# Kernel optimization log

Hardware: AMD Instinct MI355X
Metric: run time of the kernel (lower is better)

## Reference

```python
import jax, jax.numpy as jnp
import numpy as np

N_NODES = 100000
N_EDGES = 1600000
IN_DIM = 128
HID = 128
OUT = 64


def gcn_conv(x, src, dst, W, b, n_nodes):
    # x: [N, Din] -> [N, Dout]; symmetric-normalized GCN with self-loops (PyG GCNConv defaults)
    h = x @ W  # transform first (as PyG does)
    loop = jnp.arange(n_nodes, dtype=src.dtype)
    s = jnp.concatenate([src, loop])
    d = jnp.concatenate([dst, loop])
    deg = jax.ops.segment_sum(jnp.ones_like(d, dtype=h.dtype), d, num_segments=n_nodes)
    dis = jnp.where(deg > 0, jax.lax.rsqrt(deg), 0.0)
    norm = dis[s] * dis[d]  # [E+N]
    msgs = h[s] * norm[:, None]  # gather-transform
    out = jax.ops.segment_sum(msgs, d, num_segments=n_nodes)  # scatter-add
    return out + b


def setup_inputs() -> dict:
    key = jax.random.key(0)
    ks = jax.random.split(key, 12)
    x = jax.random.normal(ks[0], (N_NODES, IN_DIM), dtype=jnp.float32)
    edge_index = jax.random.randint(ks[1], (2, N_EDGES), 0, N_NODES, dtype=jnp.int32)
    def lin(k, fan_in, fan_out):
        bound = 1.0 / np.sqrt(fan_in)
        kw, kb = jax.random.split(k)
        W = jax.random.uniform(kw, (fan_in, fan_out), minval=-bound, maxval=bound, dtype=jnp.float32)
        b = jax.random.uniform(kb, (fan_out,), minval=-bound, maxval=bound, dtype=jnp.float32)
        return W, b
    W1, b1 = lin(ks[2], IN_DIM, HID)
    W2, b2 = lin(ks[3], HID, HID)
    Wp1, bp1 = lin(ks[4], HID, HID)
    Wp2, bp2 = lin(ks[5], HID, OUT)
    return {"x": x, "edge_index": edge_index,
            "W1": W1, "b1": b1, "W2": W2, "b2": b2,
            "Wp1": Wp1, "bp1": bp1, "Wp2": Wp2, "bp2": bp2}


def reference(x, edge_index, W1, b1, W2, b2, Wp1, bp1, Wp2, bp2):
    n = x.shape[0]
    src, dst = edge_index[0], edge_index[1]
    # layer 1: GCNConv + relu (dropout inactive at eval)
    h = jax.nn.relu(gcn_conv(x, src, dst, W1, b1, n))
    # layer 2
    h = jax.nn.relu(gcn_conv(h, src, dst, W2, b2, n))
    # post MLP head
    h = h @ Wp1 + bp1
    h = h @ Wp2 + bp2
    return jax.nn.log_softmax(h, axis=1)
```

## Files before the change

### kernel.cpp

```cpp
#include <hip/hip_runtime.h>
#include <hip/hip_bf16.h>
#include <cstdint>

typedef __attribute__((ext_vector_type(8))) short short8;
typedef __attribute__((ext_vector_type(16))) float f32x16;
typedef unsigned short us;

#define BIN_SHIFT 9
#define BIN_NODES 512
#define CAPB 12288
#define EPB 4096

__device__ __forceinline__ float bflo(uint32_t u) { return __builtin_bit_cast(float, u << 16); }
__device__ __forceinline__ float bfhi(uint32_t u) { return __builtin_bit_cast(float, u & 0xffff0000u); }

__device__ __forceinline__ us f32_to_bf16_rne(float f) {
  uint32_t u = __builtin_bit_cast(uint32_t, f);
  u += 0x7fffu + ((u >> 16) & 1u);
  return (us)(u >> 16);
}

__device__ __forceinline__ void split2(float f, us& h, us& l) {
  uint32_t u = __builtin_bit_cast(uint32_t, f);
  h = (us)(u >> 16);
  float fh = __builtin_bit_cast(float, u & 0xffff0000u);
  float r = f - fh;
  l = (us)(__builtin_bit_cast(uint32_t, r) >> 16);
}

__global__ __launch_bounds__(256) void k_binA(
    const int* __restrict__ src, const int* __restrict__ dst,
    uint2* __restrict__ binbuf, int* __restrict__ gcur, int E, int nbins) {
  __shared__ uint2 stage[EPB];
  __shared__ int cnt[256], base[256], cur[256], gbase[256];
  int tid = threadIdx.x;
  int e0 = blockIdx.x * EPB;
  int ne = min(EPB, E - e0);
  if (ne <= 0) return;
  cnt[tid] = 0;
  __syncthreads();
  for (int i = tid; i < ne; i += 256) atomicAdd(&cnt[dst[e0 + i] >> BIN_SHIFT], 1);
  __syncthreads();
  if (tid < 64) {
    int carry = 0;
#pragma unroll
    for (int c = 0; c < 4; ++c) {
      int v = cnt[c * 64 + tid];
      int incl = v;
#pragma unroll
      for (int off = 1; off < 64; off <<= 1) {
        int t = __shfl_up(incl, off, 64);
        if (tid >= off) incl += t;
      }
      base[c * 64 + tid] = carry + incl - v;
      carry += __shfl(incl, 63, 64);
    }
  }
  __syncthreads();
  if (tid < nbins && cnt[tid] > 0) gbase[tid] = atomicAdd(&gcur[tid], cnt[tid]);
  cur[tid] = base[tid];
  __syncthreads();
  for (int i = tid; i < ne; i += 256) {
    int d = dst[e0 + i], s = src[e0 + i];
    int p = atomicAdd(&cur[d >> BIN_SHIFT], 1);
    stage[p] = make_uint2((unsigned)d, (unsigned)s);
  }
  __syncthreads();
  for (int i = tid; i < ne; i += 256) {
    uint2 en = stage[i];
    int b = en.x >> BIN_SHIFT;
    int gi = gbase[b] + (i - base[b]);
    if (gi < CAPB) binbuf[(size_t)b * CAPB + gi] = en;
  }
}

__global__ __launch_bounds__(256) void k_passB(
    const uint2* __restrict__ binbuf, const int* __restrict__ gcur,
    int* __restrict__ deg, float* __restrict__ dis, int* __restrict__ start,
    int* __restrict__ col, int N, int nbins) {
  __shared__ int hist[512], lstart[512], cur[512];
  __shared__ int colstage[CAPB];
  __shared__ int binbase_s;
  int b = blockIdx.x, tid = threadIdx.x;
  int node0 = b << BIN_SHIFT;
  int cnt = min(gcur[b], CAPB);
  hist[tid] = 0; hist[tid + 256] = 0;
  __syncthreads();
  const uint2* bp = binbuf + (size_t)b * CAPB;
  for (int i = tid; i < cnt; i += 256) atomicAdd(&hist[bp[i].x & (BIN_NODES - 1)], 1);
  __syncthreads();
  if (tid < 64) {
    int s = 0;
    for (int i = tid; i < b; i += 64) s += min(gcur[i], CAPB);
#pragma unroll
    for (int off = 32; off; off >>= 1) s += __shfl_xor(s, off, 64);
    if (tid == 0) binbase_s = s;
    int carry = 0;
#pragma unroll
    for (int c = 0; c < 8; ++c) {
      int v = hist[c * 64 + tid];
      int incl = v;
#pragma unroll
      for (int off = 1; off < 64; off <<= 1) {
        int t = __shfl_up(incl, off, 64);
        if (tid >= off) incl += t;
      }
      lstart[c * 64 + tid] = carry + incl - v;
      carry += __shfl(incl, 63, 64);
    }
  }
  __syncthreads();
  int binbase = binbase_s;
  for (int i = tid; i < 512; i += 256) {
    int node = node0 + i;
    if (node < N) {
      int dg = hist[i];
      deg[node] = dg;
      dis[node] = rsqrtf((float)(dg + 1));
      start[node] = binbase + lstart[i];
    }
  }
  cur[tid] = lstart[tid]; cur[tid + 256] = lstart[tid + 256];
  __syncthreads();
  for (int i = tid; i < cnt; i += 256) {
    uint2 en = bp[i];
    int p = atomicAdd(&cur[en.x & (BIN_NODES - 1)], 1);
    colstage[p] = (int)en.y;
  }
  __syncthreads();
  for (int i = tid; i < cnt; i += 256) col[binbase + i] = colstage[i];
}

__global__ void k_prep(const float* __restrict__ W1, const float* __restrict__ W2,
                       const float* __restrict__ Wp1, const float* __restrict__ Wp2,
                       const float* __restrict__ bp1, const float* __restrict__ bp2,
                       us* __restrict__ Wt1h, us* __restrict__ Wt1l,
                       us* __restrict__ Wt2h, us* __restrict__ Wt2l,
                       us* __restrict__ Wch, us* __restrict__ Wcl, float* __restrict__ bc) {
  int blk = blockIdx.x, tid = threadIdx.x;
  if (blk < 128) {
    const float* W = (blk < 64) ? W1 : W2;
    us* Wh = (blk < 64) ? Wt1h : Wt2h;
    us* Wl = (blk < 64) ? Wt1l : Wt2l;
    int idx = (blk & 63) * 256 + tid;
    int k = idx >> 7, n = idx & 127;
    us h, l;
    split2(W[idx], h, l);
    Wh[n * 128 + k] = h;
    Wl[n * 128 + k] = l;
  } else if (blk < 160) {
    int idx = (blk - 128) * 256 + tid;
    int k = idx >> 6, j = idx & 63;
    float acc = 0.f;
    for (int t = 0; t < 128; ++t) acc += Wp1[k * 128 + t] * Wp2[t * 64 + j];
    us h, l;
    split2(acc, h, l);
    Wch[j * 128 + k] = h;
    Wcl[j * 128 + k] = l;
  } else {
    int j = tid;
    if (j < 64) {
      float acc = bp2[j];
      for (int t = 0; t < 128; ++t) acc += bp1[t] * Wp2[t * 64 + j];
      bc[j] = acc;
    }
  }
}

template <bool AF32>
__global__ __launch_bounds__(256) void k_gemm_mfma(
    const void* __restrict__ Av, const us* __restrict__ Wh,
    const us* __restrict__ Wl, const float* __restrict__ dis,
    us* __restrict__ out_bf16, int N, int ntiles) {
  __shared__ us As_hi[32 * 136];
  __shared__ us As_lo[32 * 136];
  int tid = threadIdx.x;
  int wave = tid >> 6, lane = tid & 63;
  int n0 = wave * 32;
  int nn = n0 + (lane & 31);
  int khalf = (lane >> 5) * 8;
  int m = lane & 31;

  short8 bh[8], bl[8];
#pragma unroll
  for (int c = 0; c < 8; ++c) {
    bh[c] = *(const short8*)&Wh[nn * 128 + c * 16 + khalf];
    bl[c] = *(const short8*)&Wl[nn * 128 + c * 16 + khalf];
  }

  for (int t = blockIdx.x; t < ntiles; t += gridDim.x) {
    int row0 = t * 32;
    __syncthreads();
    if (AF32) {
      const float* A = (const float*)Av;
      for (int j = tid; j < 1024; j += 256) {
        int r = j >> 5, c = j & 31;
        int row = row0 + r;
        float4 v = make_float4(0.f, 0.f, 0.f, 0.f);
        if (row < N) v = *(const float4*)&A[(size_t)row * 128 + c * 4];
        us h0, h1, h2, h3, l0, l1, l2, l3;
        split2(v.x, h0, l0); split2(v.y, h1, l1);
        split2(v.z, h2, l2); split2(v.w, h3, l3);
        *(ushort4*)&As_hi[r * 136 + c * 4] = make_ushort4(h0, h1, h2, h3);
        *(ushort4*)&As_lo[r * 136 + c * 4] = make_ushort4(l0, l1, l2, l3);
      }
    } else {
      const us* A = (const us*)Av;
      for (int j = tid; j < 512; j += 256) {
        int r = j >> 4, c = j & 15;
        int row = row0 + r;
        uint4 v = make_uint4(0u, 0u, 0u, 0u);
        if (row < N) v = *(const uint4*)&A[(size_t)row * 128 + c * 8];
        *(uint4*)&As_hi[r * 136 + c * 8] = v;
      }
    }
    __syncthreads();

    f32x16 acc = {};
#pragma unroll
    for (int c = 0; c < 8; ++c) {
      short8 ah = *(const short8*)&As_hi[m * 136 + c * 16 + khalf];
      acc = __builtin_amdgcn_mfma_f32_32x32x16_bf16(ah, bh[c], acc, 0, 0, 0);
      acc = __builtin_amdgcn_mfma_f32_32x32x16_bf16(ah, bl[c], acc, 0, 0, 0);
      if (AF32) {
        short8 al = *(const short8*)&As_lo[m * 136 + c * 16 + khalf];
        acc = __builtin_amdgcn_mfma_f32_32x32x16_bf16(al, bh[c], acc, 0, 0, 0);
      }
    }

    int col = n0 + (lane & 31);
    int rbase = row0 + 4 * (lane >> 5);
#pragma unroll
    for (int reg = 0; reg < 16; ++reg) {
      int row = rbase + (reg & 3) + 8 * (reg >> 2);
      if (row < N) {
        float v = acc[reg] * dis[row];
        out_bf16[(size_t)row * 128 + col] = f32_to_bf16_rne(v);
      }
    }
  }
}

__global__ __launch_bounds__(256) void k_gather(
    const us* __restrict__ h, us* __restrict__ o,
    const int* __restrict__ start, const int* __restrict__ deg,
    const int* __restrict__ col, const float* __restrict__ dis,
    const float* __restrict__ bias, int N) {
  int tid = threadIdx.x;
  int node = blockIdx.x * 8 + (tid >> 5);
  int lane = tid & 31;
  if (node >= N) return;
  const uint2* h2 = (const uint2*)h;
  uint2 u = h2[(size_t)node * 32 + lane];
  float ax = bflo(u.x), ay = bfhi(u.x), az = bflo(u.y), aw = bfhi(u.y);
  int e = start[node];
  int e_end = e + deg[node];
  for (; e + 1 < e_end; e += 2) {
    uint2 u1 = h2[(size_t)col[e] * 32 + lane];
    uint2 u2 = h2[(size_t)col[e + 1] * 32 + lane];
    ax += bflo(u1.x) + bflo(u2.x); ay += bfhi(u1.x) + bfhi(u2.x);
    az += bflo(u1.y) + bflo(u2.y); aw += bfhi(u1.y) + bfhi(u2.y);
  }
  if (e < e_end) {
    uint2 u1 = h2[(size_t)col[e] * 32 + lane];
    ax += bflo(u1.x); ay += bfhi(u1.x); az += bflo(u1.y); aw += bfhi(u1.y);
  }
  float sc = dis[node];
  float4 b = ((const float4*)bias)[lane];
  float rx = fmaxf(ax * sc + b.x, 0.f);
  float ry = fmaxf(ay * sc + b.y, 0.f);
  float rz = fmaxf(az * sc + b.z, 0.f);
  float rw = fmaxf(aw * sc + b.w, 0.f);
  uint2 po;
  po.x = ((uint32_t)f32_to_bf16_rne(ry) << 16) | f32_to_bf16_rne(rx);
  po.y = ((uint32_t)f32_to_bf16_rne(rw) << 16) | f32_to_bf16_rne(rz);
  ((uint2*)o)[(size_t)node * 32 + lane] = po;
}

__global__ __launch_bounds__(256) void k_head_mfma(
    const us* __restrict__ act, const us* __restrict__ Wch,
    const us* __restrict__ Wcl, const float* __restrict__ bc,
    float* __restrict__ out, int N) {
  __shared__ us As[64 * 136];
  __shared__ float red[2][2][64];
  int tid = threadIdx.x;
  int wave = tid >> 6, lane = tid & 63;
  int rt = wave >> 1, ct = wave & 1;
  int colj = ct * 32 + (lane & 31);
  int khalf = (lane >> 5) * 8;
  int m = lane & 31;

  short8 bh[8], bl[8];
#pragma unroll
  for (int c = 0; c < 8; ++c) {
    bh[c] = *(const short8*)&Wch[colj * 128 + c * 16 + khalf];
    bl[c] = *(const short8*)&Wcl[colj * 128 + c * 16 + khalf];
  }

  int row0 = blockIdx.x * 64;
  for (int j = tid; j < 1024; j += 256) {
    int r = j >> 4, c = j & 15;
    int row = row0 + r;
    uint4 v = make_uint4(0u, 0u, 0u, 0u);
    if (row < N) v = *(const uint4*)&act[(size_t)row * 128 + c * 8];
    *(uint4*)&As[r * 136 + c * 8] = v;
  }
  __syncthreads();

  f32x16 acc = {};
  int mrow = rt * 32 + m;
#pragma unroll
  for (int c = 0; c < 8; ++c) {
    short8 ah = *(const short8*)&As[mrow * 136 + c * 16 + khalf];
    acc = __builtin_amdgcn_mfma_f32_32x32x16_bf16(ah, bh[c], acc, 0, 0, 0);
    acc = __builtin_amdgcn_mfma_f32_32x32x16_bf16(ah, bl[c], acc, 0, 0, 0);
  }

  float bcv = bc[colj];
  float lg[16], mx[16];
#pragma unroll
  for (int reg = 0; reg < 16; ++reg) {
    lg[reg] = acc[reg] + bcv;
    float v = lg[reg];
#pragma unroll
    for (int off = 16; off > 0; off >>= 1) v = fmaxf(v, __shfl_xor(v, off, 32));
    mx[reg] = v;
  }
  if ((lane & 31) == 0) {
#pragma unroll
    for (int reg = 0; reg < 16; ++reg) {
      int rl = rt * 32 + (reg & 3) + 8 * (reg >> 2) + 4 * (lane >> 5);
      red[0][ct][rl] = mx[reg];
    }
  }
  __syncthreads();

  float ex[16], sm[16];
#pragma unroll
  for (int reg = 0; reg < 16; ++reg) {
    int rl = rt * 32 + (reg & 3) + 8 * (reg >> 2) + 4 * (lane >> 5);
    float rmax = fmaxf(red[0][0][rl], red[0][1][rl]);
    ex[reg] = lg[reg] - rmax;
    float v = expf(ex[reg]);
#pragma unroll
    for (int off = 16; off > 0; off >>= 1) v += __shfl_xor(v, off, 32);
    sm[reg] = v;
  }
  if ((lane & 31) == 0) {
#pragma unroll
    for (int reg = 0; reg < 16; ++reg) {
      int rl = rt * 32 + (reg & 3) + 8 * (reg >> 2) + 4 * (lane >> 5);
      red[1][ct][rl] = sm[reg];
    }
  }
  __syncthreads();

#pragma unroll
  for (int reg = 0; reg < 16; ++reg) {
    int rl = rt * 32 + (reg & 3) + 8 * (reg >> 2) + 4 * (lane >> 5);
    int row = row0 + rl;
    if (row < N) {
      float total = red[1][0][rl] + red[1][1][rl];
      out[(size_t)row * 64 + colj] = ex[reg] - logf(total);
    }
  }
}

extern "C" void kernel_launch(void* const* d_in, const int* in_sizes, int n_in,
                              void* d_out, int out_size, void* d_ws, size_t ws_size,
                              hipStream_t stream) {
  const float* x   = (const float*)d_in[0];
  const int*   ei  = (const int*)d_in[1];
  const float* W1  = (const float*)d_in[2];
  const float* b1  = (const float*)d_in[3];
  const float* W2  = (const float*)d_in[4];
  const float* b2  = (const float*)d_in[5];
  const float* Wp1 = (const float*)d_in[6];
  const float* bp1 = (const float*)d_in[7];
  const float* Wp2 = (const float*)d_in[8];
  const float* bp2 = (const float*)d_in[9];
  float* out = (float*)d_out;

  int N = in_sizes[0] / 128;
  int E = in_sizes[1] / 2;
  const int* src = ei;
  const int* dst = ei + E;
  int nbins = (N + BIN_NODES - 1) >> BIN_SHIFT;

  float* dis   = (float*)d_ws;
  int*   deg   = (int*)(dis + N);
  int*   start = deg + N;
  int*   col   = start + N;
  int*   gcur  = col + ((E + 3) & ~3);
  us* Wt1h = (us*)(gcur + 256);
  us* Wt1l = Wt1h + 16384;
  us* Wt2h = Wt1l + 16384;
  us* Wt2l = Wt2h + 16384;
  us* Wch  = Wt2l + 16384;
  us* Wcl  = Wch + 8192;
  float* bc = (float*)(Wcl + 8192);
  uint2* binbuf = (uint2*)(bc + 80);
  us* hbuf = (us*)(binbuf + (size_t)nbins * CAPB);
  us* act  = hbuf + (size_t)N * 128;

  hipMemsetAsync(gcur, 0, 256 * sizeof(int), stream);

  int ablocks = (E + EPB - 1) / EPB;
  k_binA<<<ablocks, 256, 0, stream>>>(src, dst, binbuf, gcur, E, nbins);
  k_passB<<<nbins, 256, 0, stream>>>(binbuf, gcur, deg, dis, start, col, N, nbins);
  k_prep<<<161, 256, 0, stream>>>(W1, W2, Wp1, Wp2, bp1, bp2,
                                  Wt1h, Wt1l, Wt2h, Wt2l, Wch, Wcl, bc);

  int ntiles = (N + 31) / 32;
  int gemm_grid = ntiles < 1024 ? ntiles : 1024;
  int agblocks = (N + 7) / 8;
  int hblocks = (N + 63) / 64;

  k_gemm_mfma<true><<<gemm_grid, 256, 0, stream>>>(x, Wt1h, Wt1l, dis, hbuf, N, ntiles);
  k_gather<<<agblocks, 256, 0, stream>>>(hbuf, act, start, deg, col, dis, b1, N);
  k_gemm_mfma<false><<<gemm_grid, 256, 0, stream>>>(act, Wt2h, Wt2l, dis, hbuf, N, ntiles);
  k_gather<<<agblocks, 256, 0, stream>>>(hbuf, act, start, deg, col, dis, b2, N);
  k_head_mfma<<<hblocks, 256, 0, stream>>>(act, Wch, Wcl, bc, out, N);
}
```

Baseline: 409.3 us.

## Fuse neighbor aggregation into following GEMM/head kernels and pack bin entries

Fuses the layer-1 gather into the layer-2 MFMA GEMM and the layer-2 gather into the output head kernel, so the aggregated activations go straight into shared memory instead of through a global buffer and extra launches. The binning pass now packs each edge into one 32-bit word (local dst in the high bits, src in the low 23 bits) and recovers the bin with a binary search over bin bases, halving bin-buffer traffic. The gather inner loop is unrolled to four neighbors. Risks: gather latency now sits inside the GEMM blocks with fewer resident waves, gemm_grid caps parallelism for the gather phase, and src indices are limited to 23 bits.

```diff
diff --git a/kernel.cpp b/kernel.cpp
--- a/kernel.cpp
+++ b/kernel.cpp
@@ -30,8 +30,8 @@
 
 __global__ __launch_bounds__(256) void k_binA(
     const int* __restrict__ src, const int* __restrict__ dst,
-    uint2* __restrict__ binbuf, int* __restrict__ gcur, int E, int nbins) {
-  __shared__ uint2 stage[EPB];
+    uint32_t* __restrict__ binbuf, int* __restrict__ gcur, int E, int nbins) {
+  __shared__ uint32_t stage[EPB];
   __shared__ int cnt[256], base[256], cur[256], gbase[256];
   int tid = threadIdx.x;
   int e0 = blockIdx.x * EPB;
@@ -63,19 +63,24 @@
   for (int i = tid; i < ne; i += 256) {
     int d = dst[e0 + i], s = src[e0 + i];
     int p = atomicAdd(&cur[d >> BIN_SHIFT], 1);
-    stage[p] = make_uint2((unsigned)d, (unsigned)s);
+    stage[p] = ((uint32_t)(d & (BIN_NODES - 1)) << 23) | (uint32_t)s;
   }
   __syncthreads();
   for (int i = tid; i < ne; i += 256) {
-    uint2 en = stage[i];
-    int b = en.x >> BIN_SHIFT;
+    uint32_t en = stage[i];
+    int lo = 0, hi = 255;
+    while (lo < hi) {
+      int mid = (lo + hi + 1) >> 1;
+      if (base[mid] <= i) lo = mid; else hi = mid - 1;
+    }
+    int b = lo;
     int gi = gbase[b] + (i - base[b]);
     if (gi < CAPB) binbuf[(size_t)b * CAPB + gi] = en;
   }
 }
 
 __global__ __launch_bounds__(256) void k_passB(
-    const uint2* __restrict__ binbuf, const int* __restrict__ gcur,
+    const uint32_t* __restrict__ binbuf, const int* __restrict__ gcur,
     int* __restrict__ deg, float* __restrict__ dis, int* __restrict__ start,
     int* __restrict__ col, int N, int nbins) {
   __shared__ int hist[512], lstart[512], cur[512];
@@ -86,8 +91,8 @@
   int cnt = min(gcur[b], CAPB);
   hist[tid] = 0; hist[tid + 256] = 0;
   __syncthreads();
-  const uint2* bp = binbuf + (size_t)b * CAPB;
-  for (int i = tid; i < cnt; i += 256) atomicAdd(&hist[bp[i].x & (BIN_NODES - 1)], 1);
+  const uint32_t* bp = binbuf + (size_t)b * CAPB;
+  for (int i = tid; i < cnt; i += 256) atomicAdd(&hist[bp[i] >> 23], 1);
   __syncthreads();
   if (tid < 64) {
     int s = 0;
@@ -123,9 +128,9 @@
   cur[tid] = lstart[tid]; cur[tid + 256] = lstart[tid + 256];
   __syncthreads();
   for (int i = tid; i < cnt; i += 256) {
-    uint2 en = bp[i];
-    int p = atomicAdd(&cur[en.x & (BIN_NODES - 1)], 1);
-    colstage[p] = (int)en.y;
+    uint32_t en = bp[i];
+    int p = atomicAdd(&cur[en >> 23], 1);
+    colstage[p] = (int)(en & 0x7fffffu);
   }
   __syncthreads();
   for (int i = tid; i < cnt; i += 256) col[binbase + i] = colstage[i];
@@ -167,9 +172,42 @@
   }
 }
 
-template <bool AF32>
+__device__ __forceinline__ uint2 gather_row(
+    const uint2* __restrict__ h2, const int* __restrict__ start,
+    const int* __restrict__ deg, const int* __restrict__ col,
+    const float* __restrict__ dis, float4 b, int node, int hl) {
+  uint2 u = h2[(size_t)node * 32 + hl];
+  float ax = bflo(u.x), ay = bfhi(u.x), az = bflo(u.y), aw = bfhi(u.y);
+  int e = start[node];
+  int e_end = e + deg[node];
+  for (; e + 3 < e_end; e += 4) {
+    int s0 = col[e], s1 = col[e + 1], s2 = col[e + 2], s3 = col[e + 3];
+    uint2 u0 = h2[(size_t)s0 * 32 + hl];
+    uint2 u1 = h2[(size_t)s1 * 32 + hl];
+    uint2 u2 = h2[(size_t)s2 * 32 + hl];
+    uint2 u3 = h2[(size_t)s3 * 32 + hl];
+    ax += (bflo(u0.x) + bflo(u1.x)) + (bflo(u2.x) + bflo(u3.x));
+    ay += (bfhi(u0.x) + bfhi(u1.x)) + (bfhi(u2.x) + bfhi(u3.x));
+    az += (bflo(u0.y) + bflo(u1.y)) + (bflo(u2.y) + bflo(u3.y));
+    aw += (bfhi(u0.y) + bfhi(u1.y)) + (bfhi(u2.y) + bfhi(u3.y));
+  }
+  for (; e < e_end; ++e) {
+    uint2 u1 = h2[(size_t)col[e] * 32 + hl];
+    ax += bflo(u1.x); ay += bfhi(u1.x); az += bflo(u1.y); aw += bfhi(u1.y);
+  }
+  float sc = dis[node];
+  float rx = fmaxf(ax * sc + b.x, 0.f);
+  float ry = fmaxf(ay * sc + b.y, 0.f);
+  float rz = fmaxf(az * sc + b.z, 0.f);
+  float rw = fmaxf(aw * sc + b.w, 0.f);
+  uint2 po;
+  po.x = ((uint32_t)f32_to_bf16_rne(ry) << 16) | f32_to_bf16_rne(rx);
+  po.y = ((uint32_t)f32_to_bf16_rne(rw) << 16) | f32_to_bf16_rne(rz);
+  return po;
+}
+
 __global__ __launch_bounds__(256) void k_gemm_mfma(
-    const void* __restrict__ Av, const us* __restrict__ Wh,
+    const float* __restrict__ A, const us* __restrict__ Wh,
     const us* __restrict__ Wl, const float* __restrict__ dis,
     us* __restrict__ out_bf16, int N, int ntiles) {
   __shared__ us As_hi[32 * 136];
@@ -191,28 +229,16 @@
   for (int t = blockIdx.x; t < ntiles; t += gridDim.x) {
     int row0 = t * 32;
     __syncthreads();
-    if (AF32) {
-      const float* A = (const float*)Av;
-      for (int j = tid; j < 1024; j += 256) {
-        int r = j >> 5, c = j & 31;
-        int row = row0 + r;
-        float4 v = make_float4(0.f, 0.f, 0.f, 0.f);
-        if (row < N) v = *(const float4*)&A[(size_t)row * 128 + c * 4];
-        us h0, h1, h2, h3, l0, l1, l2, l3;
-        split2(v.x, h0, l0); split2(v.y, h1, l1);
-        split2(v.z, h2, l2); split2(v.w, h3, l3);
-        *(ushort4*)&As_hi[r * 136 + c * 4] = make_ushort4(h0, h1, h2, h3);
-        *(ushort4*)&As_lo[r * 136 + c * 4] = make_ushort4(l0, l1, l2, l3);
-      }
-    } else {
-      const us* A = (const us*)Av;
-      for (int j = tid; j < 512; j += 256) {
-        int r = j >> 4, c = j & 15;
-        int row = row0 + r;
-        uint4 v = make_uint4(0u, 0u, 0u, 0u);
-        if (row < N) v = *(const uint4*)&A[(size_t)row * 128 + c * 8];
-        *(uint4*)&As_hi[r * 136 + c * 8] = v;
-      }
+    for (int j = tid; j < 1024; j += 256) {
+      int r = j >> 5, c = j & 31;
+      int row = row0 + r;
+      float4 v = make_float4(0.f, 0.f, 0.f, 0.f);
+      if (row < N) v = *(const float4*)&A[(size_t)row * 128 + c * 4];
+      us h0, h1, h2, h3, l0, l1, l2, l3;
+      split2(v.x, h0, l0); split2(v.y, h1, l1);
+      split2(v.z, h2, l2); split2(v.w, h3, l3);
+      *(ushort4*)&As_hi[r * 136 + c * 4] = make_ushort4(h0, h1, h2, h3);
+      *(ushort4*)&As_lo[r * 136 + c * 4] = make_ushort4(l0, l1, l2, l3);
     }
     __syncthreads();
 
@@ -220,66 +246,88 @@
 #pragma unroll
     for (int c = 0; c < 8; ++c) {
       short8 ah = *(const short8*)&As_hi[m * 136 + c * 16 + khalf];
+      short8 al = *(const short8*)&As_lo[m * 136 + c * 16 + khalf];
       acc = __builtin_amdgcn_mfma_f32_32x32x16_bf16(ah, bh[c], acc, 0, 0, 0);
       acc = __builtin_amdgcn_mfma_f32_32x32x16_bf16(ah, bl[c], acc, 0, 0, 0);
-      if (AF32) {
-        short8 al = *(const short8*)&As_lo[m * 136 + c * 16 + khalf];
-        acc = __builtin_amdgcn_mfma_f32_32x32x16_bf16(al, bh[c], acc, 0, 0, 0);
-      }
-    }
-
-    int col = n0 + (lane & 31);
+      acc = __builtin_amdgcn_mfma_f32_32x32x16_bf16(al, bh[c], acc, 0, 0, 0);
+    }
+
+    int colj = n0 + (lane & 31);
     int rbase = row0 + 4 * (lane >> 5);
 #pragma unroll
     for (int reg = 0; reg < 16; ++reg) {
       int row = rbase + (reg & 3) + 8 * (reg >> 2);
       if (row < N) {
         float v = acc[reg] * dis[row];
-        out_bf16[(size_t)row * 128 + col] = f32_to_bf16_rne(v);
+        out_bf16[(size_t)row * 128 + colj] = f32_to_bf16_rne(v);
       }
     }
   }
 }
 
-__global__ __launch_bounds__(256) void k_gather(
-    const us* __restrict__ h, us* __restrict__ o,
+__global__ __launch_bounds__(256) void k_gg(
+    const us* __restrict__ h, const us* __restrict__ Wh, const us* __restrict__ Wl,
     const int* __restrict__ start, const int* __restrict__ deg,
     const int* __restrict__ col, const float* __restrict__ dis,
-    const float* __restrict__ bias, int N) {
+    const float* __restrict__ bias, us* __restrict__ out_bf16, int N, int ntiles) {
+  __shared__ us As[32 * 136];
   int tid = threadIdx.x;
-  int node = blockIdx.x * 8 + (tid >> 5);
-  int lane = tid & 31;
-  if (node >= N) return;
+  int wave = tid >> 6, lane = tid & 63;
+  int n0 = wave * 32;
+  int nn = n0 + (lane & 31);
+  int khalf = (lane >> 5) * 8;
+  int m = lane & 31;
+  int hw = tid >> 5, hl = tid & 31;
+
+  short8 bh[8], bl[8];
+#pragma unroll
+  for (int c = 0; c < 8; ++c) {
+    bh[c] = *(const short8*)&Wh[nn * 128 + c * 16 + khalf];
+    bl[c] = *(const short8*)&Wl[nn * 128 + c * 16 + khalf];
+  }
+
   const uint2* h2 = (const uint2*)h;
-  uint2 u = h2[(size_t)node * 32 + lane];
-  float ax = bflo(u.x), ay = bfhi(u.x), az = bflo(u.y), aw = bfhi(u.y);
-  int e = start[node];
-  int e_end = e + deg[node];
-  for (; e + 1 < e_end; e += 2) {
-    uint2 u1 = h2[(size_t)col[e] * 32 + lane];
-    uint2 u2 = h2[(size_t)col[e + 1] * 32 + lane];
-    ax += bflo(u1.x) + bflo(u2.x); ay += bfhi(u1.x) + bfhi(u2.x);
-    az += bflo(u1.y) + bflo(u2.y); aw += bfhi(u1.y) + bfhi(u2.y);
-  }
-  if (e < e_end) {
-    uint2 u1 = h2[(size_t)col[e] * 32 + lane];
-    ax += bflo(u1.x); ay += bfhi(u1.x); az += bflo(u1.y); aw += bfhi(u1.y);
-  }
-  float sc = dis[node];
-  float4 b = ((const float4*)bias)[lane];
-  float rx = fmaxf(ax * sc + b.x, 0.f);
-  float ry = fmaxf(ay * sc + b.y, 0.f);
-  float rz = fmaxf(az * sc + b.z, 0.f);
-  float rw = fmaxf(aw * sc + b.w, 0.f);
-  uint2 po;
-  po.x = ((uint32_t)f32_to_bf16_rne(ry) << 16) | f32_to_bf16_rne(rx);
-  po.y = ((uint32_t)f32_to_bf16_rne(rw) << 16) | f32_to_bf16_rne(rz);
-  ((uint2*)o)[(size_t)node * 32 + lane] = po;
-}
-
-__global__ __launch_bounds__(256) void k_head_mfma(
-    const us* __restrict__ act, const us* __restrict__ Wch,
-    const us* __restrict__ Wcl, const float* __restrict__ bc,
+  float4 b = ((const float4*)bias)[hl];
+
+  for (int t = blockIdx.x; t < ntiles; t += gridDim.x) {
+    int row0 = t * 32;
+    __syncthreads();
+#pragma unroll
+    for (int i = 0; i < 4; ++i) {
+      int r = hw * 4 + i;
+      int node = row0 + r;
+      uint2 po = make_uint2(0u, 0u);
+      if (node < N) po = gather_row(h2, start, deg, col, dis, b, node, hl);
+      *(uint2*)&As[r * 136 + hl * 4] = po;
+    }
+    __syncthreads();
+
+    f32x16 acc = {};
+#pragma unroll
+    for (int c = 0; c < 8; ++c) {
+      short8 ah = *(const short8*)&As[m * 136 + c * 16 + khalf];
+      acc = __builtin_amdgcn_mfma_f32_32x32x16_bf16(ah, bh[c], acc, 0, 0, 0);
+      acc = __builtin_amdgcn_mfma_f32_32x32x16_bf16(ah, bl[c], acc, 0, 0, 0);
+    }
+
+    int colj = n0 + (lane & 31);
+    int rbase = row0 + 4 * (lane >> 5);
+#pragma unroll
+    for (int reg = 0; reg < 16; ++reg) {
+      int row = rbase + (reg & 3) + 8 * (reg >> 2);
+      if (row < N) {
+        float v = acc[reg] * dis[row];
+        out_bf16[(size_t)row * 128 + colj] = f32_to_bf16_rne(v);
+      }
+    }
+  }
+}
+
+__global__ __launch_bounds__(256) void k_gh(
+    const us* __restrict__ h, const us* __restrict__ Wch, const us* __restrict__ Wcl,
+    const int* __restrict__ start, const int* __restrict__ deg,
+    const int* __restrict__ col, const float* __restrict__ dis,
+    const float* __restrict__ bias, const float* __restrict__ bc,
     float* __restrict__ out, int N) {
   __shared__ us As[64 * 136];
   __shared__ float red[2][2][64];
@@ -289,6 +337,7 @@
   int colj = ct * 32 + (lane & 31);
   int khalf = (lane >> 5) * 8;
   int m = lane & 31;
+  int hw = tid >> 5, hl = tid & 31;
 
   short8 bh[8], bl[8];
 #pragma unroll
@@ -297,13 +346,17 @@
     bl[c] = *(const short8*)&Wcl[colj * 128 + c * 16 + khalf];
   }
 
+  const uint2* h2 = (const uint2*)h;
+  float4 b = ((const float4*)bias)[hl];
   int row0 = blockIdx.x * 64;
-  for (int j = tid; j < 1024; j += 256) {
-    int r = j >> 4, c = j & 15;
-    int row = row0 + r;
-    uint4 v = make_uint4(0u, 0u, 0u, 0u);
-    if (row < N) v = *(const uint4*)&act[(size_t)row * 128 + c * 8];
-    *(uint4*)&As[r * 136 + c * 8] = v;
+
+#pragma unroll
+  for (int i = 0; i < 8; ++i) {
+    int r = hw * 8 + i;
+    int node = row0 + r;
+    uint2 po = make_uint2(0u, 0u);
+    if (node < N) po = gather_row(h2, start, deg, col, dis, b, node, hl);
+    *(uint2*)&As[r * 136 + hl * 4] = po;
   }
   __syncthreads();
 
@@ -399,9 +452,9 @@
   us* Wch  = Wt2l + 16384;
   us* Wcl  = Wch + 8192;
   float* bc = (float*)(Wcl + 8192);
-  uint2* binbuf = (uint2*)(bc + 80);
-  us* hbuf = (us*)(binbuf + (size_t)nbins * CAPB);
-  us* act  = hbuf + (size_t)N * 128;
+  uint32_t* binbuf = (uint32_t*)(bc + 80);
+  us* hbuf  = (us*)(binbuf + (size_t)nbins * CAPB);
+  us* hbuf2 = hbuf + (size_t)N * 128;
 
   hipMemsetAsync(gcur, 0, 256 * sizeof(int), stream);
 
@@ -413,12 +466,10 @@
 
   int ntiles = (N + 31) / 32;
   int gemm_grid = ntiles < 1024 ? ntiles : 1024;
-  int agblocks = (N + 7) / 8;
   int hblocks = (N + 63) / 64;
 
-  k_gemm_mfma<true><<<gemm_grid, 256, 0, stream>>>(x, Wt1h, Wt1l, dis, hbuf, N, ntiles);
-  k_gather<<<agblocks, 256, 0, stream>>>(hbuf, act, start, deg, col, dis, b1, N);
-  k_gemm_mfma<false><<<gemm_grid, 256, 0, stream>>>(act, Wt2h, Wt2l, dis, hbuf, N, ntiles);
-  k_gather<<<agblocks, 256, 0, stream>>>(hbuf, act, start, deg, col, dis, b2, N);
-  k_head_mfma<<<hblocks, 256, 0, stream>>>(act, Wch, Wcl, bc, out, N);
-}
+  k_gemm_mfma<<<gemm_grid, 256, 0, stream>>>(x, Wt1h, Wt1l, dis, hbuf, N, ntiles);
+  k_gg<<<gemm_grid, 256, 0, stream>>>(hbuf, Wt2h, Wt2l, start, deg, col, dis, b1,
+                                      hbuf2, N, ntiles);
+  k_gh<<<hblocks, 256, 0, stream>>>(hbuf2, Wch, Wcl, start, deg, col, dis, b2, bc, out, N);
+}
```

After: 520.3 us. 1.27x slower.
